# Optimization experiments

Measured on AMD Instinct MI355X. Metric: run time of the kernel, lower is better.

Reference implementation:

```python
import jax, jax.numpy as jnp
import numpy as np

FEATS = 1024
HEAD = 16
DH = FEATS // HEAD
B, N = 2, 2048
SQRT_D = FEATS ** 0.5  # note: source scales by sqrt(feats), not sqrt(head_dim)


def setup_inputs() -> dict:
    key = jax.random.key(0)
    ks = jax.random.split(key, 9)
    s = 1.0 / np.sqrt(FEATS)
    return {
        "x": jax.random.normal(ks[0], (B, N, FEATS), dtype=jnp.float32),
        "Wq": jax.random.normal(ks[1], (FEATS, FEATS), dtype=jnp.float32) * s,
        "bq": jax.random.normal(ks[2], (FEATS,), dtype=jnp.float32) * s,
        "Wk": jax.random.normal(ks[3], (FEATS, FEATS), dtype=jnp.float32) * s,
        "bk": jax.random.normal(ks[4], (FEATS,), dtype=jnp.float32) * s,
        "Wv": jax.random.normal(ks[5], (FEATS, FEATS), dtype=jnp.float32) * s,
        "bv": jax.random.normal(ks[6], (FEATS,), dtype=jnp.float32) * s,
        "Wo": jax.random.normal(ks[7], (FEATS, FEATS), dtype=jnp.float32) * s,
        "bo": jax.random.normal(ks[8], (FEATS,), dtype=jnp.float32) * s,
    }


def reference(x, Wq, bq, Wk, bk, Wv, bv, Wo, bo):
    b, n, f = x.shape
    # Linear layers: y = x @ W^T + b (torch nn.Linear convention)
    q = (x @ Wq.T + bq).reshape(b, n, HEAD, DH).transpose(0, 2, 1, 3)  # bhnd
    k = (x @ Wk.T + bk).reshape(b, n, HEAD, DH).transpose(0, 2, 1, 3)
    v = (x @ Wv.T + bv).reshape(b, n, HEAD, DH).transpose(0, 2, 1, 3)
    score = jax.nn.softmax(jnp.einsum('bhif,bhjf->bhij', q, k) / SQRT_D, axis=-1)
    attn = jnp.einsum('bhij,bhjf->bihf', score, v)  # [b, n, head, dh]
    o = attn.reshape(b, n, f) @ Wo.T + bo
    return o
```

## Files before the change

### kernel.cpp

```cpp
#include <hip/hip_runtime.h>
#include <stdint.h>

typedef short short8 __attribute__((ext_vector_type(8)));
typedef float f32x4 __attribute__((ext_vector_type(4)));
typedef float f32x16 __attribute__((ext_vector_type(16)));
typedef unsigned int uint2v __attribute__((ext_vector_type(2)));
typedef unsigned int uint4v __attribute__((ext_vector_type(4)));

#define SEQ 2048
#define NBH 32

__device__ __forceinline__ unsigned short f32_to_bf16(float f) {
  union { float f; uint32_t u; } v; v.f = f;
  return (unsigned short)((v.u + 0x7fffu + ((v.u >> 16) & 1u)) >> 16);
}

__device__ __forceinline__ float bf16_to_f32(unsigned short u) {
  union { uint32_t u; float f; } v; v.u = ((uint32_t)u) << 16;
  return v.f;
}

__device__ __forceinline__ unsigned int cvtpk_bf16(float lo, float hi) {
  unsigned int r;
  asm("v_cvt_pk_bf16_f32 %0, %1, %2" : "=v"(r) : "v"(lo), "v"(hi));
  return r;
}

__device__ __forceinline__ void gload_lds16(const unsigned short* g, unsigned short* l) {
  __builtin_amdgcn_global_load_lds(
      (const __attribute__((address_space(1))) unsigned int*)g,
      (__attribute__((address_space(3))) unsigned int*)l, 16, 0, 0);
}

__global__ void cast_f32_bf16(const float* __restrict__ in,
                              unsigned short* __restrict__ out, int n4) {
  int i = blockIdx.x * blockDim.x + threadIdx.x;
  if (i >= n4) return;
  float4 v = ((const float4*)in)[i];
  ushort4 o;
  o.x = f32_to_bf16(v.x); o.y = f32_to_bf16(v.y);
  o.z = f32_to_bf16(v.z); o.w = f32_to_bf16(v.w);
  ((ushort4*)out)[i] = o;
}

#define GSWZ(row, k) ((k) ^ ((row) & 3) ^ (((row) >> 2) & 3))

__device__ __forceinline__ void gemm_core_1024(
    const unsigned short* __restrict__ Ag,
    const unsigned short* __restrict__ Bg,
    int tid, f32x4 acc[4][4])
{
  __shared__ __align__(16) unsigned short As[128 * 32];
  __shared__ __align__(16) unsigned short Bs[128 * 32];
  const int w = tid >> 6, l = tid & 63;
  const int wr = w >> 1, wc = w & 1;
  const int lc = l & 15, lg = l >> 4;

  const int c0row = tid >> 2,        c0ks = tid & 3;
  const int c1row = (256 + tid) >> 2;

  for (int k0 = 0; k0 < 1024; k0 += 32) {
    int kg0 = GSWZ(c0row, c0ks);
    int kg1 = GSWZ(c1row, c0ks);
    gload_lds16(Ag + (size_t)c0row * 1024 + k0 + kg0 * 8, As + (w * 64) * 8);
    gload_lds16(Ag + (size_t)c1row * 1024 + k0 + kg1 * 8, As + (256 + w * 64) * 8);
    gload_lds16(Bg + (size_t)c0row * 1024 + k0 + kg0 * 8, Bs + (w * 64) * 8);
    gload_lds16(Bg + (size_t)c1row * 1024 + k0 + kg1 * 8, Bs + (256 + w * 64) * 8);
    __syncthreads();

    short8 a[4], b[4];
#pragma unroll
    for (int mi = 0; mi < 4; ++mi) {
      int row = wr * 64 + mi * 16 + lc;
      int ko = GSWZ(row, lg);
      a[mi] = *(const short8*)(As + row * 32 + ko * 8);
    }
#pragma unroll
    for (int ni = 0; ni < 4; ++ni) {
      int row = wc * 64 + ni * 16 + lc;
      int ko = GSWZ(row, lg);
      b[ni] = *(const short8*)(Bs + row * 32 + ko * 8);
    }
#pragma unroll
    for (int mi = 0; mi < 4; ++mi)
#pragma unroll
      for (int ni = 0; ni < 4; ++ni)
        acc[mi][ni] = __builtin_amdgcn_mfma_f32_16x16x32_bf16(a[mi], b[ni], acc[mi][ni], 0, 0, 0);
    __syncthreads();
  }
}

__global__ __launch_bounds__(256, 2)
void gemm_qkv(const unsigned short* __restrict__ XB,
              const unsigned short* __restrict__ WQB,
              const unsigned short* __restrict__ WKB,
              const unsigned short* __restrict__ WVB,
              const float* __restrict__ bq,
              const float* __restrict__ bk,
              const float* __restrict__ bv,
              unsigned short* __restrict__ Qo,
              unsigned short* __restrict__ Ko,
              unsigned short* __restrict__ Vo)
{
  const int tid = threadIdx.x;
  const int tm = blockIdx.x * 128;
  const int tn = blockIdx.y * 128;
  const int wi = tn >> 10;
  const int tnl = tn & 1023;
  const unsigned short* Bw = (wi == 0 ? WQB : wi == 1 ? WKB : WVB) + (size_t)tnl * 1024;
  const float* bias = (wi == 0 ? bq : wi == 1 ? bk : bv);
  unsigned short* Out = (wi == 0 ? Qo : wi == 1 ? Ko : Vo);
  const float qscale = (wi == 0) ? 0.04508422002778011f : 1.0f;

  f32x4 acc[4][4];
#pragma unroll
  for (int mi = 0; mi < 4; ++mi)
#pragma unroll
    for (int ni = 0; ni < 4; ++ni)
      acc[mi][ni] = (f32x4){0.f, 0.f, 0.f, 0.f};

  gemm_core_1024(XB + (size_t)tm * 1024, Bw, tid, acc);

  const int w = tid >> 6, l = tid & 63;
  const int wr = w >> 1, wc = w & 1;
  const int lc = l & 15, lg = l >> 4;
#pragma unroll
  for (int ni = 0; ni < 4; ++ni) {
    int nl = tnl + wc * 64 + ni * 16 + lc;
    float bb = bias[nl];
    int h = nl >> 6, d = nl & 63;
#pragma unroll
    for (int mi = 0; mi < 4; ++mi) {
#pragma unroll
      for (int r = 0; r < 4; ++r) {
        int m = tm + wr * 64 + mi * 16 + lg * 4 + r;
        int b = m >> 11, i = m & 2047;
        float v = (acc[mi][ni][r] + bb) * qscale;
        Out[(((size_t)(b * 16 + h) * SEQ + i) << 6) + d] = f32_to_bf16(v);
      }
    }
  }
}

__global__ __launch_bounds__(256, 2)
void gemm_o(const unsigned short* __restrict__ AT,
            const unsigned short* __restrict__ WOB,
            const float* __restrict__ bo,
            float* __restrict__ Of)
{
  const int tid = threadIdx.x;
  const int tm = blockIdx.x * 128;
  const int tn = blockIdx.y * 128;

  f32x4 acc[4][4];
#pragma unroll
  for (int mi = 0; mi < 4; ++mi)
#pragma unroll
    for (int ni = 0; ni < 4; ++ni)
      acc[mi][ni] = (f32x4){0.f, 0.f, 0.f, 0.f};

  gemm_core_1024(AT + (size_t)tm * 1024, WOB + (size_t)tn * 1024, tid, acc);

  const int w = tid >> 6, l = tid & 63;
  const int wr = w >> 1, wc = w & 1;
  const int lc = l & 15, lg = l >> 4;
#pragma unroll
  for (int ni = 0; ni < 4; ++ni) {
    int n = tn + wc * 64 + ni * 16 + lc;
    float bb = bo[n];
#pragma unroll
    for (int mi = 0; mi < 4; ++mi) {
#pragma unroll
      for (int r = 0; r < 4; ++r) {
        int m = tm + wr * 64 + mi * 16 + lg * 4 + r;
        Of[(size_t)m * 1024 + n] = acc[mi][ni][r] + bb;
      }
    }
  }
}

__global__ void transpose_v(const unsigned short* __restrict__ V,
                            unsigned short* __restrict__ VT)
{
  __shared__ unsigned short tile[32][33];
  int bh = blockIdx.z;
  int n0 = blockIdx.x * 32, d0 = blockIdx.y * 32;
  int x = threadIdx.x;
  for (int yy = threadIdx.y; yy < 32; yy += 8)
    tile[yy][x] = V[((size_t)bh * SEQ + n0 + yy) * 64 + d0 + x];
  __syncthreads();
  for (int yy = threadIdx.y; yy < 32; yy += 8)
    VT[((size_t)bh * 64 + d0 + yy) * SEQ + n0 + x] = tile[x][yy];
}

__global__ __launch_bounds__(256, 4)
void attn_fwd7(const unsigned short* __restrict__ Qm,
               const unsigned short* __restrict__ Km,
               const unsigned short* __restrict__ VTm,
               unsigned short* __restrict__ Op0,
               unsigned short* __restrict__ Op1,
               float* __restrict__ Lp)
{
  __shared__ __align__(16) unsigned short KV[2][64 * 128];
  const int tid = threadIdx.x, w = tid >> 6, l = tid & 63;
  const int lq = l & 31, hi = l >> 5;
  const int m15 = lq & 15;
  const int bh = blockIdx.x, q0 = blockIdx.y * 128;
  const int js = blockIdx.z;
  const int j0 = js << 10;

  const unsigned short* Qb = Qm + ((size_t)bh * SEQ + q0 + w * 32) * 64;
  const unsigned short* Kg = Km + ((size_t)bh * SEQ + j0) * 64;
  const unsigned short* Vg = VTm + (size_t)bh * 64 * SEQ + j0;

  const int sr = l >> 4;
  const int ss = l & 15;
  const unsigned short* sp[4];
  int sstep[4];
#pragma unroll
  for (int i = 0; i < 4; ++i) {
    int r = w * 16 + i * 4 + sr;
    int t = ss ^ (i * 4 + sr);
    if (t < 8) { sp[i] = Kg + (size_t)r * 64 + t * 8;          sstep[i] = 64 * 64; }
    else       { sp[i] = Vg + (size_t)r * SEQ + (t - 8) * 8;   sstep[i] = 64; }
  }

  short8 qf[4];
#pragma unroll
  for (int kc = 0; kc < 4; ++kc)
    qf[kc] = *(const short8*)(Qb + lq * 64 + kc * 16 + hi * 8);

  f32x16 o0, o1;
#pragma unroll
  for (int r = 0; r < 16; ++r) { o0[r] = 0.f; o1[r] = 0.f; }
  float sm[8];
#pragma unroll
  for (int i = 0; i < 8; ++i) sm[i] = 0.f;

#pragma unroll
  for (int i = 0; i < 4; ++i) {
    gload_lds16(sp[i], &KV[0][(w * 16 + i * 4) * 128]);
    sp[i] += sstep[i];
  }
  __syncthreads();

  for (int t = 0; t < 16; ++t) {
    const int cur = t & 1;
    if (t + 1 < 16) {
#pragma unroll
      for (int i = 0; i < 4; ++i) {
        gload_lds16(sp[i], &KV[cur ^ 1][(w * 16 + i * 4) * 128]);
        sp[i] += sstep[i];
      }
    }
    const char* Tb = (const char*)(&KV[cur][0]);

    f32x16 s0, s1;
#pragma unroll
    for (int r = 0; r < 16; ++r) { s0[r] = 0.f; s1[r] = 0.f; }
    __builtin_amdgcn_s_setprio(1);
#pragma unroll
    for (int kc = 0; kc < 4; ++kc) {
      short8 kf = *(const short8*)(Tb + lq * 256 + (((kc * 2 + hi) ^ m15) << 4));
      s0 = __builtin_amdgcn_mfma_f32_32x32x16_bf16(kf, qf[kc], s0, 0, 0, 0);
    }
#pragma unroll
    for (int kc = 0; kc < 4; ++kc) {
      short8 kf = *(const short8*)(Tb + (32 + lq) * 256 + (((kc * 2 + hi) ^ m15) << 4));
      s1 = __builtin_amdgcn_mfma_f32_32x32x16_bf16(kf, qf[kc], s1, 0, 0, 0);
    }
    __builtin_amdgcn_s_setprio(0);

    float p[32];
#pragma unroll
    for (int r = 0; r < 16; ++r) {
      p[r] = __builtin_amdgcn_exp2f(s0[r]);
      p[16 + r] = __builtin_amdgcn_exp2f(s1[r]);
    }
#pragma unroll
    for (int i = 0; i < 8; ++i)
      sm[i] += (p[i] + p[i + 8]) + (p[i + 16] + p[i + 24]);

    short8 pa[4];
#pragma unroll
    for (int ks = 0; ks < 4; ++ks) {
      const int pb = ks * 8;
      unsigned int a0 = cvtpk_bf16(p[pb + 0], p[pb + 1]);
      unsigned int a1 = cvtpk_bf16(p[pb + 2], p[pb + 3]);
      unsigned int b0 = cvtpk_bf16(p[pb + 4], p[pb + 5]);
      unsigned int b1 = cvtpk_bf16(p[pb + 6], p[pb + 7]);
      unsigned int a0x = __shfl_xor((int)a0, 32), b0x = __shfl_xor((int)b0, 32);
      unsigned int a1x = __shfl_xor((int)a1, 32), b1x = __shfl_xor((int)b1, 32);
      union { uint4v u; short8 s; } cvt;
      cvt.u.x = hi ? b0x : a0;
      cvt.u.y = hi ? b1x : a1;
      cvt.u.z = hi ? b0 : a0x;
      cvt.u.w = hi ? b1 : a1x;
      pa[ks] = cvt.s;
    }

    __builtin_amdgcn_s_setprio(1);
#pragma unroll
    for (int ks = 0; ks < 4; ++ks) {
      short8 vf = *(const short8*)(Tb + lq * 256 + (((8 + ks * 2 + hi) ^ m15) << 4));
      o0 = __builtin_amdgcn_mfma_f32_32x32x16_bf16(vf, pa[ks], o0, 0, 0, 0);
    }
#pragma unroll
    for (int ks = 0; ks < 4; ++ks) {
      short8 vf = *(const short8*)(Tb + (32 + lq) * 256 + (((8 + ks * 2 + hi) ^ m15) << 4));
      o1 = __builtin_amdgcn_mfma_f32_32x32x16_bf16(vf, pa[ks], o1, 0, 0, 0);
    }
    __builtin_amdgcn_s_setprio(0);
    __syncthreads();
  }

  float lden = ((sm[0] + sm[1]) + (sm[2] + sm[3])) + ((sm[4] + sm[5]) + (sm[6] + sm[7]));
  lden += __shfl_xor(lden, 32);
  const int b = bh >> 4, h = bh & 15;
  const int iq = q0 + w * 32 + lq;
  unsigned short* Op = js ? Op1 : Op0;
  if (hi == 0) Lp[(size_t)js * (NBH * SEQ) + (size_t)bh * SEQ + iq] = lden;
  const size_t obase = ((size_t)b * SEQ + iq) * 1024 + h * 64;
#pragma unroll
  for (int rq = 0; rq < 4; ++rq) {
    uint2v pk0, pk1;
    pk0.x = cvtpk_bf16(o0[rq * 4 + 0], o0[rq * 4 + 1]);
    pk0.y = cvtpk_bf16(o0[rq * 4 + 2], o0[rq * 4 + 3]);
    pk1.x = cvtpk_bf16(o1[rq * 4 + 0], o1[rq * 4 + 1]);
    pk1.y = cvtpk_bf16(o1[rq * 4 + 2], o1[rq * 4 + 3]);
    *(uint2v*)(Op + obase + rq * 8 + hi * 4) = pk0;
    *(uint2v*)(Op + obase + 32 + rq * 8 + hi * 4) = pk1;
  }
}

__global__ __launch_bounds__(256)
void attn_norm(const unsigned short* __restrict__ Op0,
               const unsigned short* __restrict__ Op1,
               const float* __restrict__ Lp,
               unsigned short* __restrict__ ATB)
{
  const int b = blockIdx.y;
  const int g = blockIdx.x * 256 + threadIdx.x;
  const size_t gi = (size_t)b * 524288 + g;
  const ushort4 a = ((const ushort4*)Op0)[gi];
  const ushort4 c = ((const ushort4*)Op1)[gi];
  const int e = g << 2;
  const int i = e >> 10, col = e & 1023, h = col >> 6;
  const size_t lix = (size_t)((b << 4) + h) * SEQ + i;
  const float inv = 1.0f / (Lp[lix] + Lp[(size_t)NBH * SEQ + lix]);
  ushort4 o;
  o.x = f32_to_bf16((bf16_to_f32(a.x) + bf16_to_f32(c.x)) * inv);
  o.y = f32_to_bf16((bf16_to_f32(a.y) + bf16_to_f32(c.y)) * inv);
  o.z = f32_to_bf16((bf16_to_f32(a.z) + bf16_to_f32(c.z)) * inv);
  o.w = f32_to_bf16((bf16_to_f32(a.w) + bf16_to_f32(c.w)) * inv);
  ((ushort4*)ATB)[gi] = o;
}

extern "C" void kernel_launch(void* const* d_in, const int* in_sizes, int n_in,
                              void* d_out, int out_size, void* d_ws, size_t ws_size,
                              hipStream_t stream) {
  (void)in_sizes; (void)n_in; (void)out_size; (void)ws_size;
  const float* x  = (const float*)d_in[0];
  const float* Wq = (const float*)d_in[1];
  const float* bq = (const float*)d_in[2];
  const float* Wk = (const float*)d_in[3];
  const float* bk = (const float*)d_in[4];
  const float* Wv = (const float*)d_in[5];
  const float* bv = (const float*)d_in[6];
  const float* Wo = (const float*)d_in[7];
  const float* bo = (const float*)d_in[8];
  float* Of = (float*)d_out;

  unsigned short* ws  = (unsigned short*)d_ws;
  unsigned short* XB  = ws;
  unsigned short* WQB = ws + 4194304u;
  unsigned short* WKB = ws + 5242880u;
  unsigned short* WVB = ws + 6291456u;
  unsigned short* WOB = ws + 7340032u;
  unsigned short* QB  = ws + 8388608u;
  unsigned short* KB  = ws + 12582912u;
  unsigned short* VB  = ws + 16777216u;
  unsigned short* VTB = ws + 20971520u;
  unsigned short* ATB = ws + 25165824u;
  unsigned short* Op0 = ws;
  unsigned short* Op1 = ws + 16777216u;
  float* Lp = (float*)(ws + 4194304u);

  cast_f32_bf16<<<4096, 256, 0, stream>>>(x,  XB,  1048576);
  cast_f32_bf16<<<1024, 256, 0, stream>>>(Wq, WQB, 262144);
  cast_f32_bf16<<<1024, 256, 0, stream>>>(Wk, WKB, 262144);
  cast_f32_bf16<<<1024, 256, 0, stream>>>(Wv, WVB, 262144);
  cast_f32_bf16<<<1024, 256, 0, stream>>>(Wo, WOB, 262144);

  gemm_qkv<<<dim3(32, 24), 256, 0, stream>>>(XB, WQB, WKB, WVB, bq, bk, bv, QB, KB, VB);
  transpose_v<<<dim3(64, 2, 32), dim3(32, 8), 0, stream>>>(VB, VTB);

  attn_fwd7<<<dim3(32, 16, 2), 256, 0, stream>>>(QB, KB, VTB, Op0, Op1, Lp);
  attn_norm<<<dim3(2048, 2), 256, 0, stream>>>(Op0, Op1, Lp, ATB);
  gemm_o<<<dim3(32, 8), 256, 0, stream>>>(ATB, WOB, bo, Of);
}
```

Before: 132.4 us.

## Fuse V transpose into QKV GEMM epilogue and retile output projection

The QKV GEMM epilogue now writes V directly in transposed (d-major) layout using packed bf16 stores, which removes the separate transpose_v kernel and its extra read/write pass over V. The output projection GEMM uses 64x128 tiles with its own single-buffered LDS loop, so it launches twice as many blocks (512 instead of 256) for better CU fill. The trade-offs are strided 8-byte stores for V and a smaller per-block tile with less data reuse in gemm_o.

```diff
diff --git a/kernel.cpp b/kernel.cpp
--- a/kernel.cpp
+++ b/kernel.cpp
@@ -100,7 +100,7 @@
               const float* __restrict__ bv,
               unsigned short* __restrict__ Qo,
               unsigned short* __restrict__ Ko,
-              unsigned short* __restrict__ Vo)
+              unsigned short* __restrict__ VTo)
 {
   const int tid = threadIdx.x;
   const int tm = blockIdx.x * 128;
@@ -109,7 +109,6 @@
   const int tnl = tn & 1023;
   const unsigned short* Bw = (wi == 0 ? WQB : wi == 1 ? WKB : WVB) + (size_t)tnl * 1024;
   const float* bias = (wi == 0 ? bq : wi == 1 ? bk : bv);
-  unsigned short* Out = (wi == 0 ? Qo : wi == 1 ? Ko : Vo);
   const float qscale = (wi == 0) ? 0.04508422002778011f : 1.0f;
 
   f32x4 acc[4][4];
@@ -124,19 +123,39 @@
   const int w = tid >> 6, l = tid & 63;
   const int wr = w >> 1, wc = w & 1;
   const int lc = l & 15, lg = l >> 4;
-#pragma unroll
-  for (int ni = 0; ni < 4; ++ni) {
-    int nl = tnl + wc * 64 + ni * 16 + lc;
-    float bb = bias[nl];
-    int h = nl >> 6, d = nl & 63;
-#pragma unroll
-    for (int mi = 0; mi < 4; ++mi) {
-#pragma unroll
-      for (int r = 0; r < 4; ++r) {
-        int m = tm + wr * 64 + mi * 16 + lg * 4 + r;
-        int b = m >> 11, i = m & 2047;
-        float v = (acc[mi][ni][r] + bb) * qscale;
-        Out[(((size_t)(b * 16 + h) * SEQ + i) << 6) + d] = f32_to_bf16(v);
+
+  if (wi == 2) {
+#pragma unroll
+    for (int ni = 0; ni < 4; ++ni) {
+      int nl = tnl + wc * 64 + ni * 16 + lc;
+      float bb = bias[nl];
+      int h = nl >> 6, d = nl & 63;
+#pragma unroll
+      for (int mi = 0; mi < 4; ++mi) {
+        int ibase = tm + wr * 64 + mi * 16 + lg * 4;
+        int b = ibase >> 11, i = ibase & 2047;
+        uint2v pk;
+        pk.x = cvtpk_bf16(acc[mi][ni][0] + bb, acc[mi][ni][1] + bb);
+        pk.y = cvtpk_bf16(acc[mi][ni][2] + bb, acc[mi][ni][3] + bb);
+        *(uint2v*)(VTo + (((size_t)(b * 16 + h) * 64 + d) * SEQ + i)) = pk;
+      }
+    }
+  } else {
+    unsigned short* Out = (wi == 0) ? Qo : Ko;
+#pragma unroll
+    for (int ni = 0; ni < 4; ++ni) {
+      int nl = tnl + wc * 64 + ni * 16 + lc;
+      float bb = bias[nl];
+      int h = nl >> 6, d = nl & 63;
+#pragma unroll
+      for (int mi = 0; mi < 4; ++mi) {
+#pragma unroll
+        for (int r = 0; r < 4; ++r) {
+          int m = tm + wr * 64 + mi * 16 + lg * 4 + r;
+          int b = m >> 11, i = m & 2047;
+          float v = (acc[mi][ni][r] + bb) * qscale;
+          Out[(((size_t)(b * 16 + h) * SEQ + i) << 6) + d] = f32_to_bf16(v);
+        }
       }
     }
   }
@@ -148,49 +167,64 @@
             const float* __restrict__ bo,
             float* __restrict__ Of)
 {
+  __shared__ __align__(16) unsigned short As[64 * 32];
+  __shared__ __align__(16) unsigned short Bs[128 * 32];
   const int tid = threadIdx.x;
-  const int tm = blockIdx.x * 128;
+  const int w = tid >> 6, l = tid & 63;
+  const int lc = l & 15, lg = l >> 4;
+  const int tm = blockIdx.x * 64;
   const int tn = blockIdx.y * 128;
-
-  f32x4 acc[4][4];
+  const unsigned short* Ag = AT + (size_t)tm * 1024;
+  const unsigned short* Bg = WOB + (size_t)tn * 1024;
+
+  const int crow = tid >> 2, cks = tid & 3;
+
+  f32x4 acc[4][2];
 #pragma unroll
   for (int mi = 0; mi < 4; ++mi)
 #pragma unroll
-    for (int ni = 0; ni < 4; ++ni)
+    for (int ni = 0; ni < 2; ++ni)
       acc[mi][ni] = (f32x4){0.f, 0.f, 0.f, 0.f};
 
-  gemm_core_1024(AT + (size_t)tm * 1024, WOB + (size_t)tn * 1024, tid, acc);
-
-  const int w = tid >> 6, l = tid & 63;
-  const int wr = w >> 1, wc = w & 1;
-  const int lc = l & 15, lg = l >> 4;
-#pragma unroll
-  for (int ni = 0; ni < 4; ++ni) {
-    int n = tn + wc * 64 + ni * 16 + lc;
+  for (int k0 = 0; k0 < 1024; k0 += 32) {
+    int kg = GSWZ(crow, cks);
+    gload_lds16(Ag + (size_t)crow * 1024 + k0 + kg * 8, As + w * 512);
+    gload_lds16(Bg + (size_t)crow * 1024 + k0 + kg * 8, Bs + w * 512);
+    gload_lds16(Bg + (size_t)(64 + crow) * 1024 + k0 + kg * 8, Bs + 2048 + w * 512);
+    __syncthreads();
+
+    short8 a[4], b[2];
+#pragma unroll
+    for (int mi = 0; mi < 4; ++mi) {
+      int row = mi * 16 + lc;
+      a[mi] = *(const short8*)(As + row * 32 + GSWZ(row, lg) * 8);
+    }
+#pragma unroll
+    for (int ni = 0; ni < 2; ++ni) {
+      int row = w * 32 + ni * 16 + lc;
+      b[ni] = *(const short8*)(Bs + row * 32 + GSWZ(row, lg) * 8);
+    }
+#pragma unroll
+    for (int mi = 0; mi < 4; ++mi)
+#pragma unroll
+      for (int ni = 0; ni < 2; ++ni)
+        acc[mi][ni] = __builtin_amdgcn_mfma_f32_16x16x32_bf16(a[mi], b[ni], acc[mi][ni], 0, 0, 0);
+    __syncthreads();
+  }
+
+#pragma unroll
+  for (int ni = 0; ni < 2; ++ni) {
+    int n = tn + w * 32 + ni * 16 + lc;
     float bb = bo[n];
 #pragma unroll
     for (int mi = 0; mi < 4; ++mi) {
 #pragma unroll
       for (int r = 0; r < 4; ++r) {
-        int m = tm + wr * 64 + mi * 16 + lg * 4 + r;
+        int m = tm + mi * 16 + lg * 4 + r;
         Of[(size_t)m * 1024 + n] = acc[mi][ni][r] + bb;
       }
     }
   }
-}
-
-__global__ void transpose_v(const unsigned short* __restrict__ V,
-                            unsigned short* __restrict__ VT)
-{
-  __shared__ unsigned short tile[32][33];
-  int bh = blockIdx.z;
-  int n0 = blockIdx.x * 32, d0 = blockIdx.y * 32;
-  int x = threadIdx.x;
-  for (int yy = threadIdx.y; yy < 32; yy += 8)
-    tile[yy][x] = V[((size_t)bh * SEQ + n0 + yy) * 64 + d0 + x];
-  __syncthreads();
-  for (int yy = threadIdx.y; yy < 32; yy += 8)
-    VT[((size_t)bh * 64 + d0 + yy) * SEQ + n0 + x] = tile[x][yy];
 }
 
 __global__ __launch_bounds__(256, 4)
@@ -379,7 +413,6 @@
   unsigned short* WOB = ws + 7340032u;
   unsigned short* QB  = ws + 8388608u;
   unsigned short* KB  = ws + 12582912u;
-  unsigned short* VB  = ws + 16777216u;
   unsigned short* VTB = ws + 20971520u;
   unsigned short* ATB = ws + 25165824u;
   unsigned short* Op0 = ws;
@@ -392,10 +425,9 @@
   cast_f32_bf16<<<1024, 256, 0, stream>>>(Wv, WVB, 262144);
   cast_f32_bf16<<<1024, 256, 0, stream>>>(Wo, WOB, 262144);
 
-  gemm_qkv<<<dim3(32, 24), 256, 0, stream>>>(XB, WQB, WKB, WVB, bq, bk, bv, QB, KB, VB);
-  transpose_v<<<dim3(64, 2, 32), dim3(32, 8), 0, stream>>>(VB, VTB);
+  gemm_qkv<<<dim3(32, 24), 256, 0, stream>>>(XB, WQB, WKB, WVB, bq, bk, bv, QB, KB, VTB);
 
   attn_fwd7<<<dim3(32, 16, 2), 256, 0, stream>>>(QB, KB, VTB, Op0, Op1, Lp);
   attn_norm<<<dim3(2048, 2), 256, 0, stream>>>(Op0, Op1, Lp, ATB);
-  gemm_o<<<dim3(32, 8), 256, 0, stream>>>(ATB, WOB, bo, Of);
-}
+  gemm_o<<<dim3(64, 8), 256, 0, stream>>>(ATB, WOB, bo, Of);
+}
```

Measured after the change: 125.3 us. 1.06x faster.
